# Performance work log

Hardware: AMD Instinct MI355X
Metric: run time of the kernel (lower is better)

Reference implementation:

```python
import jax, jax.numpy as jnp
import numpy as np

WINDOW = 16
NUM_HEADS = 4
DIM = 256
LN_EPS = 1e-5


def setup_inputs() -> dict:
    key = jax.random.key(0)
    ks = jax.random.split(key, 8)
    B, C, N = 8, DIM, 16384
    s = 1.0 / np.sqrt(C)
    x = jax.random.normal(ks[0], (B, C, N), dtype=jnp.float32)
    in_proj_w = jax.random.uniform(ks[1], (3 * C, C), minval=-s, maxval=s, dtype=jnp.float32)
    in_proj_b = jnp.zeros((3 * C,), dtype=jnp.float32)
    out_proj_w = jax.random.uniform(ks[2], (C, C), minval=-s, maxval=s, dtype=jnp.float32)
    out_proj_b = jnp.zeros((C,), dtype=jnp.float32)
    ln_g = jnp.ones((C,), dtype=jnp.float32)
    ln_b = jnp.zeros((C,), dtype=jnp.float32)
    return {"x": x, "in_proj_w": in_proj_w, "in_proj_b": in_proj_b,
            "out_proj_w": out_proj_w, "out_proj_b": out_proj_b,
            "ln_g": ln_g, "ln_b": ln_b}


def _swin_attn_1d(x, in_proj_w, in_proj_b, out_proj_w, out_proj_b, ln_g, ln_b):
    B, C, N = x.shape
    W = WINDOW
    H = NUM_HEADS
    hd = C // H
    xt = jnp.transpose(x, (0, 2, 1))                      # [B, N, C]
    pad_len = (W - N % W) % W                             # static Python int
    if pad_len > 0:
        xt = jnp.pad(xt, ((0, 0), (0, pad_len), (0, 0)))
    N_pad = N + pad_len
    nw = B * (N_pad // W)
    xw = xt.reshape(nw, W, C)                             # [nw, W, C]
    # QKV projection (torch MHA: x @ in_proj_w.T + in_proj_b)
    qkv = jnp.einsum('nwc,dc->nwd', xw, in_proj_w) + in_proj_b  # [nw, W, 3C]
    q, k, v = jnp.split(qkv, 3, axis=-1)
    q = q.reshape(nw, W, H, hd) * (1.0 / np.sqrt(hd))
    k = k.reshape(nw, W, H, hd)
    v = v.reshape(nw, W, H, hd)
    scores = jnp.einsum('nqhd,nkhd->nhqk', q, k)          # [nw, H, W, W]
    probs = jax.nn.softmax(scores, axis=-1)
    attn = jnp.einsum('nhqk,nkhd->nqhd', probs, v).reshape(nw, W, C)
    attn = jnp.einsum('nwc,dc->nwd', attn, out_proj_w) + out_proj_b
    # residual + LayerNorm
    y = attn + xw
    mu = jnp.mean(y, axis=-1, keepdims=True)
    var = jnp.mean(jnp.square(y - mu), axis=-1, keepdims=True)
    y = (y - mu) * jax.lax.rsqrt(var + LN_EPS) * ln_g + ln_b
    y = y.reshape(B, N_pad, C)
    if pad_len > 0:
        y = y[:, :N, :]
    return jnp.transpose(y, (0, 2, 1))                    # [B, C, N]


def reference(x, in_proj_w, in_proj_b, out_proj_w, out_proj_b, ln_g, ln_b):
    return _swin_attn_1d(x, in_proj_w, in_proj_b, out_proj_w, out_proj_b, ln_g, ln_b)
```

## Files before the change

kernel.cpp:

```cpp
#include <hip/hip_runtime.h>


#define C_DIM 256
#define NSEQ  16384

typedef __attribute__((ext_vector_type(8))) short bf16x8;
typedef __attribute__((ext_vector_type(4))) float f32x4;

__device__ __forceinline__ unsigned short f2bf(float f) {
    unsigned int u = __builtin_bit_cast(unsigned int, f);
    u += 0x7FFFu + ((u >> 16) & 1u);
    return (unsigned short)(u >> 16);
}
__device__ __forceinline__ float bf2f(unsigned short h) {
    unsigned int u = ((unsigned int)h) << 16;
    return __builtin_bit_cast(float, u);
}
__device__ __forceinline__ unsigned int pack2(float a, float b) {
    return ((unsigned int)f2bf(b) << 16) | (unsigned int)f2bf(a);
}
__device__ __forceinline__ uint2 pack4(f32x4 v) {
    uint2 r; r.x = pack2(v[0], v[1]); r.y = pack2(v[2], v[3]); return r;
}
__device__ __forceinline__ int xsw(int row, int col) {
    return col ^ (((row >> 3) & 1) << 4);
}

__global__ void prep_weights(const float* __restrict__ wq_f, const float* __restrict__ wo_f,
                             unsigned short* __restrict__ wq, unsigned short* __restrict__ wo) {
    int i = blockIdx.x * 256 + threadIdx.x;
    if (i < 768 * 256) {
        int nt = i >> 12, r = i & 4095;
        int k = r >> 9, r2 = r & 511;
        int l = r2 >> 5, r3 = r2 & 31;
        wq[i] = f2bf(wq_f[(nt * 16 + l) * 256 + k * 32 + r3]);
    }
    if (i < 256 * 256) {
        int nt = i >> 12, r = i & 4095;
        int k = r >> 9, r2 = r & 511;
        int l = r2 >> 5, r3 = r2 & 31;
        wo[i] = f2bf(wo_f[(nt * 16 + l) * 256 + k * 32 + r3]);
    }
}

__global__ __launch_bounds__(1024, 4) void swin_fused(
    const float* __restrict__ x,
    const unsigned short* __restrict__ wq,
    const unsigned short* __restrict__ wo,
    const float* __restrict__ bq,
    const float* __restrict__ bo,
    const float* __restrict__ lng,
    const float* __restrict__ lnb,
    float* __restrict__ out)
{
    __shared__ __align__(16) unsigned short lds_x[64][264];
    __shared__ __align__(16) unsigned short lds_qk[64][520];
    __shared__ __align__(16) unsigned short lds_vt[256][72];
    __shared__ __align__(16) unsigned short lds_p[16][16][16];
    __shared__ float lds_mean[64];
    __shared__ float lds_rstd[64];

    const int tid  = threadIdx.x;
    const int wv   = tid >> 6;
    const int lane = tid & 63;
    const int l15  = lane & 15;
    const int quad = lane >> 4;

    const int w0    = blockIdx.x * 4;
    const int batch = w0 >> 10;
    const int nbase = (w0 & 1023) << 4;
    const long xbase = (long)batch * ((long)C_DIM * NSEQ) + nbase;

    {
        const int t4 = (tid & 15) << 2;
        const int c4 = (tid >> 4) << 2;
        float4 r[4];
        #pragma unroll
        for (int j = 0; j < 4; ++j)
            r[j] = *reinterpret_cast<const float4*>(&x[xbase + (long)(c4 + j) * NSEQ + t4]);
        const float* rf = reinterpret_cast<const float*>(r);
        #pragma unroll
        for (int i = 0; i < 4; ++i) {
            uint2 v;
            v.x = pack2(rf[0 * 4 + i], rf[1 * 4 + i]);
            v.y = pack2(rf[2 * 4 + i], rf[3 * 4 + i]);
            *reinterpret_cast<uint2*>(&lds_x[t4 + i][xsw(t4 + i, c4)]) = v;
        }
    }

    const unsigned short* wqbase = wq + l15 * 32 + quad * 8;
    bf16x8 wA[8], wB[8];
    #pragma unroll
    for (int k = 0; k < 8; ++k)
        wA[k] = *reinterpret_cast<const bf16x8*>(wqbase + wv * 4096 + k * 512);

    __syncthreads();

    {
        #pragma unroll
        for (int k = 0; k < 8; ++k)
            wB[k] = *reinterpret_cast<const bf16x8*>(wqbase + (16 + wv) * 4096 + k * 512);
        const float4 b4 = *reinterpret_cast<const float4*>(&bq[wv * 16 + quad * 4]);
        f32x4 acc[4];
        #pragma unroll
        for (int s = 0; s < 4; ++s) acc[s] = {b4.x, b4.y, b4.z, b4.w};
        #pragma unroll
        for (int k = 0; k < 8; ++k) {
            #pragma unroll
            for (int s = 0; s < 4; ++s) {
                const int row = s * 16 + l15;
                bf16x8 a = *reinterpret_cast<const bf16x8*>(&lds_x[row][xsw(row, k * 32 + quad * 8)]);
                acc[s] = __builtin_amdgcn_mfma_f32_16x16x32_bf16(wA[k], a, acc[s], 0, 0, 0);
            }
        }
        const int cb = wv * 16 + quad * 4;
        #pragma unroll
        for (int s = 0; s < 4; ++s) {
            const int row = s * 16 + l15;
            *reinterpret_cast<uint2*>(&lds_qk[row][xsw(row, cb)]) = pack4(acc[s]);
        }
    }
    {
        #pragma unroll
        for (int k = 0; k < 8; ++k)
            wA[k] = *reinterpret_cast<const bf16x8*>(wqbase + (32 + wv) * 4096 + k * 512);
        const float4 b4 = *reinterpret_cast<const float4*>(&bq[256 + wv * 16 + quad * 4]);
        f32x4 acc[4];
        #pragma unroll
        for (int s = 0; s < 4; ++s) acc[s] = {b4.x, b4.y, b4.z, b4.w};
        #pragma unroll
        for (int k = 0; k < 8; ++k) {
            #pragma unroll
            for (int s = 0; s < 4; ++s) {
                const int row = s * 16 + l15;
                bf16x8 a = *reinterpret_cast<const bf16x8*>(&lds_x[row][xsw(row, k * 32 + quad * 8)]);
                acc[s] = __builtin_amdgcn_mfma_f32_16x16x32_bf16(wB[k], a, acc[s], 0, 0, 0);
            }
        }
        const int cb = 256 + wv * 16 + quad * 4;
        #pragma unroll
        for (int s = 0; s < 4; ++s) {
            const int row = s * 16 + l15;
            *reinterpret_cast<uint2*>(&lds_qk[row][xsw(row, cb)]) = pack4(acc[s]);
        }
    }
    {
        const float bias = bq[512 + wv * 16 + l15];
        f32x4 acc[4];
        #pragma unroll
        for (int s = 0; s < 4; ++s) acc[s] = {bias, bias, bias, bias};
        #pragma unroll
        for (int k = 0; k < 8; ++k) {
            #pragma unroll
            for (int s = 0; s < 4; ++s) {
                const int row = s * 16 + l15;
                bf16x8 a = *reinterpret_cast<const bf16x8*>(&lds_x[row][xsw(row, k * 32 + quad * 8)]);
                acc[s] = __builtin_amdgcn_mfma_f32_16x16x32_bf16(a, wA[k], acc[s], 0, 0, 0);
            }
        }
        #pragma unroll
        for (int s = 0; s < 4; ++s)
            *reinterpret_cast<uint2*>(&lds_vt[wv * 16 + l15][s * 16 + quad * 4]) = pack4(acc[s]);
    }
    __syncthreads();

    {
        const int g = wv >> 2;
        const int h = wv & 3;
        const int row = g * 16 + l15;
        f32x4 sc = {0.f, 0.f, 0.f, 0.f};
        #pragma unroll
        for (int kk = 0; kk < 2; ++kk) {
            bf16x8 aq = *reinterpret_cast<const bf16x8*>(&lds_qk[row][xsw(row, h * 64 + kk * 32 + quad * 8)]);
            bf16x8 bk = *reinterpret_cast<const bf16x8*>(&lds_qk[row][xsw(row, 256 + h * 64 + kk * 32 + quad * 8)]);
            sc = __builtin_amdgcn_mfma_f32_16x16x32_bf16(aq, bk, sc, 0, 0, 0);
        }
        #pragma unroll
        for (int r = 0; r < 4; ++r) {
            float s = sc[r] * 0.125f;
            float m = s;
            #pragma unroll
            for (int msk = 1; msk <= 8; msk <<= 1) m = fmaxf(m, __shfl_xor(m, msk, 16));
            float e = __expf(s - m);
            float su = e;
            #pragma unroll
            for (int msk = 1; msk <= 8; msk <<= 1) su += __shfl_xor(su, msk, 16);
            lds_p[wv][quad * 4 + r][l15] = f2bf(e / su);
        }
        bf16x8 ap = {0,0,0,0,0,0,0,0};
        if (quad < 2) ap = *reinterpret_cast<const bf16x8*>(&lds_p[wv][l15][quad * 8]);
        #pragma unroll
        for (int dt = 0; dt < 4; ++dt) {
            bf16x8 bv = {0,0,0,0,0,0,0,0};
            if (quad < 2)
                bv = *reinterpret_cast<const bf16x8*>(&lds_vt[h * 64 + dt * 16 + l15][g * 16 + quad * 8]);
            f32x4 acc = {0.f, 0.f, 0.f, 0.f};
            acc = __builtin_amdgcn_mfma_f32_16x16x32_bf16(bv, ap, acc, 0, 0, 0);
            const int cb = h * 64 + dt * 16 + quad * 4;
            *reinterpret_cast<uint2*>(&lds_qk[row][xsw(row, cb)]) = pack4(acc);
        }
    }

    const unsigned short* wobase = wo + l15 * 32 + quad * 8;
    #pragma unroll
    for (int k = 0; k < 8; ++k)
        wA[k] = *reinterpret_cast<const bf16x8*>(wobase + wv * 4096 + k * 512);

    __syncthreads();

    unsigned short* ldy = &lds_vt[0][0];
    {
        const float4 b4 = *reinterpret_cast<const float4*>(&bo[wv * 16 + quad * 4]);
        f32x4 acc[4];
        #pragma unroll
        for (int s = 0; s < 4; ++s) acc[s] = {b4.x, b4.y, b4.z, b4.w};
        #pragma unroll
        for (int k = 0; k < 8; ++k) {
            #pragma unroll
            for (int s = 0; s < 4; ++s) {
                const int row = s * 16 + l15;
                bf16x8 a = *reinterpret_cast<const bf16x8*>(&lds_qk[row][xsw(row, k * 32 + quad * 8)]);
                acc[s] = __builtin_amdgcn_mfma_f32_16x16x32_bf16(wA[k], a, acc[s], 0, 0, 0);
            }
        }
        const int cb = wv * 16 + quad * 4;
        #pragma unroll
        for (int s = 0; s < 4; ++s) {
            const int row = s * 16 + l15;
            uint2 xr = *reinterpret_cast<const uint2*>(&lds_x[row][xsw(row, cb)]);
            f32x4 y;
            y[0] = acc[s][0] + bf2f((unsigned short)(xr.x & 0xffff));
            y[1] = acc[s][1] + bf2f((unsigned short)(xr.x >> 16));
            y[2] = acc[s][2] + bf2f((unsigned short)(xr.y & 0xffff));
            y[3] = acc[s][3] + bf2f((unsigned short)(xr.y >> 16));
            *reinterpret_cast<uint2*>(&ldy[row * 264 + xsw(row, cb)]) = pack4(y);
        }
    }
    __syncthreads();

    {
        const int row = tid >> 4, part = tid & 15;
        float s = 0.f, sq = 0.f;
        #pragma unroll
        for (int half = 0; half < 2; ++half) {
            bf16x8 yv = *reinterpret_cast<const bf16x8*>(&ldy[row * 264 + xsw(row, part * 16 + half * 8)]);
            #pragma unroll
            for (int ii = 0; ii < 8; ++ii) {
                float v = bf2f((unsigned short)yv[ii]);
                s += v; sq += v * v;
            }
        }
        #pragma unroll
        for (int msk = 1; msk <= 8; msk <<= 1) {
            s  += __shfl_xor(s,  msk, 16);
            sq += __shfl_xor(sq, msk, 16);
        }
        if (part == 0) {
            float mean = s * (1.0f / 256.0f);
            float var  = sq * (1.0f / 256.0f) - mean * mean;
            lds_mean[row] = mean;
            lds_rstd[row] = rsqrtf(var + 1e-5f);
        }
    }
    __syncthreads();

    {
        const int t4 = (tid & 15) << 2;
        const int c0 = tid >> 4;
        float mean[4], rstd[4];
        #pragma unroll
        for (int i = 0; i < 4; ++i) { mean[i] = lds_mean[t4 + i]; rstd[i] = lds_rstd[t4 + i]; }
        #pragma unroll
        for (int it = 0; it < 4; ++it) {
            const int c = c0 + (it << 6);
            const float g = lng[c], b = lnb[c];
            float4 o;
            float* of = reinterpret_cast<float*>(&o);
            #pragma unroll
            for (int i = 0; i < 4; ++i)
                of[i] = (bf2f(ldy[(t4 + i) * 264 + xsw(t4 + i, c)]) - mean[i]) * rstd[i] * g + b;
            *reinterpret_cast<float4*>(&out[xbase + (long)c * NSEQ + t4]) = o;
        }
    }
}

extern "C" void kernel_launch(void* const* d_in, const int* in_sizes, int n_in,
                              void* d_out, int out_size, void* d_ws, size_t ws_size,
                              hipStream_t stream) {
    const float* x   = (const float*)d_in[0];
    const float* ipw = (const float*)d_in[1];
    const float* ipb = (const float*)d_in[2];
    const float* opw = (const float*)d_in[3];
    const float* opb = (const float*)d_in[4];
    const float* lng = (const float*)d_in[5];
    const float* lnb = (const float*)d_in[6];
    float* out = (float*)d_out;

    unsigned short* wq = (unsigned short*)d_ws;
    unsigned short* wo = wq + 768 * 256;

    prep_weights<<<768, 256, 0, stream>>>(ipw, opw, wq, wo);
    swin_fused<<<2048, 1024, 0, stream>>>(x, wq, wo, ipb, opb, lng, lnb, out);
}
```

Before: 352.4 us.

## Re-tile projection GEMMs so each wave keeps activation fragments in registers

Changes how the QKV and output projections are split across the 16 waves. Each wave now owns 32 rows (sp) and loops over several 16-column weight tiles (j + 8t), holding the activation fragments for its rows in registers. Before, each wave owned one weight tile and re-read all 64 rows from LDS for every k step. This cuts LDS reads of x and of the attention output, but it raises register pressure (16 bf16x8 activation fragments plus 8 weight fragments) and makes each wave reload weight tiles from global memory more often.

```diff
diff --git a/kernel.cpp b/kernel.cpp
--- a/kernel.cpp
+++ b/kernel.cpp
@@ -65,19 +65,24 @@
     const int lane = tid & 63;
     const int l15  = lane & 15;
     const int quad = lane >> 4;
+    const int sp   = wv & 1;
+    const int j    = wv >> 1;
 
     const int w0    = blockIdx.x * 4;
     const int batch = w0 >> 10;
     const int nbase = (w0 & 1023) << 4;
     const long xbase = (long)batch * ((long)C_DIM * NSEQ) + nbase;
 
+    const int rowA = sp * 32 + l15;
+    const int rowB = sp * 32 + 16 + l15;
+
     {
         const int t4 = (tid & 15) << 2;
         const int c4 = (tid >> 4) << 2;
         float4 r[4];
         #pragma unroll
-        for (int j = 0; j < 4; ++j)
-            r[j] = *reinterpret_cast<const float4*>(&x[xbase + (long)(c4 + j) * NSEQ + t4]);
+        for (int jj = 0; jj < 4; ++jj)
+            r[jj] = *reinterpret_cast<const float4*>(&x[xbase + (long)(c4 + jj) * NSEQ + t4]);
         const float* rf = reinterpret_cast<const float*>(r);
         #pragma unroll
         for (int i = 0; i < 4; ++i) {
@@ -89,78 +94,57 @@
     }
 
     const unsigned short* wqbase = wq + l15 * 32 + quad * 8;
-    bf16x8 wA[8], wB[8];
+    bf16x8 w[8];
     #pragma unroll
     for (int k = 0; k < 8; ++k)
-        wA[k] = *reinterpret_cast<const bf16x8*>(wqbase + wv * 4096 + k * 512);
-
-    __syncthreads();
-
-    {
+        w[k] = *reinterpret_cast<const bf16x8*>(wqbase + j * 4096 + k * 512);
+
+    __syncthreads();
+
+    bf16x8 xaA[8], xaB[8];
+    #pragma unroll
+    for (int k = 0; k < 8; ++k) {
+        xaA[k] = *reinterpret_cast<const bf16x8*>(&lds_x[rowA][xsw(rowA, k * 32 + quad * 8)]);
+        xaB[k] = *reinterpret_cast<const bf16x8*>(&lds_x[rowB][xsw(rowB, k * 32 + quad * 8)]);
+    }
+
+    #pragma unroll
+    for (int t = 0; t < 4; ++t) {
+        const int nt = j + 8 * t;
+        if (t) {
+            #pragma unroll
+            for (int k = 0; k < 8; ++k)
+                w[k] = *reinterpret_cast<const bf16x8*>(wqbase + nt * 4096 + k * 512);
+        }
+        const float4 b4 = *reinterpret_cast<const float4*>(&bq[nt * 16 + quad * 4]);
+        f32x4 accA = {b4.x, b4.y, b4.z, b4.w};
+        f32x4 accB = accA;
+        #pragma unroll
+        for (int k = 0; k < 8; ++k) {
+            accA = __builtin_amdgcn_mfma_f32_16x16x32_bf16(w[k], xaA[k], accA, 0, 0, 0);
+            accB = __builtin_amdgcn_mfma_f32_16x16x32_bf16(w[k], xaB[k], accB, 0, 0, 0);
+        }
+        const int cb = nt * 16 + quad * 4;
+        *reinterpret_cast<uint2*>(&lds_qk[rowA][xsw(rowA, cb)]) = pack4(accA);
+        *reinterpret_cast<uint2*>(&lds_qk[rowB][xsw(rowB, cb)]) = pack4(accB);
+    }
+    #pragma unroll
+    for (int t = 4; t < 6; ++t) {
+        const int nt = j + 8 * t;
         #pragma unroll
         for (int k = 0; k < 8; ++k)
-            wB[k] = *reinterpret_cast<const bf16x8*>(wqbase + (16 + wv) * 4096 + k * 512);
-        const float4 b4 = *reinterpret_cast<const float4*>(&bq[wv * 16 + quad * 4]);
-        f32x4 acc[4];
-        #pragma unroll
-        for (int s = 0; s < 4; ++s) acc[s] = {b4.x, b4.y, b4.z, b4.w};
+            w[k] = *reinterpret_cast<const bf16x8*>(wqbase + nt * 4096 + k * 512);
+        const float bias = bq[nt * 16 + l15];
+        f32x4 accA = {bias, bias, bias, bias};
+        f32x4 accB = accA;
         #pragma unroll
         for (int k = 0; k < 8; ++k) {
-            #pragma unroll
-            for (int s = 0; s < 4; ++s) {
-                const int row = s * 16 + l15;
-                bf16x8 a = *reinterpret_cast<const bf16x8*>(&lds_x[row][xsw(row, k * 32 + quad * 8)]);
-                acc[s] = __builtin_amdgcn_mfma_f32_16x16x32_bf16(wA[k], a, acc[s], 0, 0, 0);
-            }
-        }
-        const int cb = wv * 16 + quad * 4;
-        #pragma unroll
-        for (int s = 0; s < 4; ++s) {
-            const int row = s * 16 + l15;
-            *reinterpret_cast<uint2*>(&lds_qk[row][xsw(row, cb)]) = pack4(acc[s]);
-        }
-    }
-    {
-        #pragma unroll
-        for (int k = 0; k < 8; ++k)
-            wA[k] = *reinterpret_cast<const bf16x8*>(wqbase + (32 + wv) * 4096 + k * 512);
-        const float4 b4 = *reinterpret_cast<const float4*>(&bq[256 + wv * 16 + quad * 4]);
-        f32x4 acc[4];
-        #pragma unroll
-        for (int s = 0; s < 4; ++s) acc[s] = {b4.x, b4.y, b4.z, b4.w};
-        #pragma unroll
-        for (int k = 0; k < 8; ++k) {
-            #pragma unroll
-            for (int s = 0; s < 4; ++s) {
-                const int row = s * 16 + l15;
-                bf16x8 a = *reinterpret_cast<const bf16x8*>(&lds_x[row][xsw(row, k * 32 + quad * 8)]);
-                acc[s] = __builtin_amdgcn_mfma_f32_16x16x32_bf16(wB[k], a, acc[s], 0, 0, 0);
-            }
-        }
-        const int cb = 256 + wv * 16 + quad * 4;
-        #pragma unroll
-        for (int s = 0; s < 4; ++s) {
-            const int row = s * 16 + l15;
-            *reinterpret_cast<uint2*>(&lds_qk[row][xsw(row, cb)]) = pack4(acc[s]);
-        }
-    }
-    {
-        const float bias = bq[512 + wv * 16 + l15];
-        f32x4 acc[4];
-        #pragma unroll
-        for (int s = 0; s < 4; ++s) acc[s] = {bias, bias, bias, bias};
-        #pragma unroll
-        for (int k = 0; k < 8; ++k) {
-            #pragma unroll
-            for (int s = 0; s < 4; ++s) {
-                const int row = s * 16 + l15;
-                bf16x8 a = *reinterpret_cast<const bf16x8*>(&lds_x[row][xsw(row, k * 32 + quad * 8)]);
-                acc[s] = __builtin_amdgcn_mfma_f32_16x16x32_bf16(a, wA[k], acc[s], 0, 0, 0);
-            }
-        }
-        #pragma unroll
-        for (int s = 0; s < 4; ++s)
-            *reinterpret_cast<uint2*>(&lds_vt[wv * 16 + l15][s * 16 + quad * 4]) = pack4(acc[s]);
+            accA = __builtin_amdgcn_mfma_f32_16x16x32_bf16(xaA[k], w[k], accA, 0, 0, 0);
+            accB = __builtin_amdgcn_mfma_f32_16x16x32_bf16(xaB[k], w[k], accB, 0, 0, 0);
+        }
+        const int vr = (nt - 32) * 16 + l15;
+        *reinterpret_cast<uint2*>(&lds_vt[vr][sp * 32 + quad * 4])      = pack4(accA);
+        *reinterpret_cast<uint2*>(&lds_vt[vr][sp * 32 + 16 + quad * 4]) = pack4(accB);
     }
     __syncthreads();
 
@@ -204,36 +188,53 @@
     const unsigned short* wobase = wo + l15 * 32 + quad * 8;
     #pragma unroll
     for (int k = 0; k < 8; ++k)
-        wA[k] = *reinterpret_cast<const bf16x8*>(wobase + wv * 4096 + k * 512);
+        w[k] = *reinterpret_cast<const bf16x8*>(wobase + j * 4096 + k * 512);
 
     __syncthreads();
 
     unsigned short* ldy = &lds_vt[0][0];
     {
-        const float4 b4 = *reinterpret_cast<const float4*>(&bo[wv * 16 + quad * 4]);
-        f32x4 acc[4];
-        #pragma unroll
-        for (int s = 0; s < 4; ++s) acc[s] = {b4.x, b4.y, b4.z, b4.w};
+        bf16x8 aaA[8], aaB[8];
         #pragma unroll
         for (int k = 0; k < 8; ++k) {
-            #pragma unroll
-            for (int s = 0; s < 4; ++s) {
-                const int row = s * 16 + l15;
-                bf16x8 a = *reinterpret_cast<const bf16x8*>(&lds_qk[row][xsw(row, k * 32 + quad * 8)]);
-                acc[s] = __builtin_amdgcn_mfma_f32_16x16x32_bf16(wA[k], a, acc[s], 0, 0, 0);
-            }
-        }
-        const int cb = wv * 16 + quad * 4;
-        #pragma unroll
-        for (int s = 0; s < 4; ++s) {
-            const int row = s * 16 + l15;
-            uint2 xr = *reinterpret_cast<const uint2*>(&lds_x[row][xsw(row, cb)]);
-            f32x4 y;
-            y[0] = acc[s][0] + bf2f((unsigned short)(xr.x & 0xffff));
-            y[1] = acc[s][1] + bf2f((unsigned short)(xr.x >> 16));
-            y[2] = acc[s][2] + bf2f((unsigned short)(xr.y & 0xffff));
-            y[3] = acc[s][3] + bf2f((unsigned short)(xr.y >> 16));
-            *reinterpret_cast<uint2*>(&ldy[row * 264 + xsw(row, cb)]) = pack4(y);
+            aaA[k] = *reinterpret_cast<const bf16x8*>(&lds_qk[rowA][xsw(rowA, k * 32 + quad * 8)]);
+            aaB[k] = *reinterpret_cast<const bf16x8*>(&lds_qk[rowB][xsw(rowB, k * 32 + quad * 8)]);
+        }
+        #pragma unroll
+        for (int t = 0; t < 2; ++t) {
+            const int nt = j + 8 * t;
+            if (t) {
+                #pragma unroll
+                for (int k = 0; k < 8; ++k)
+                    w[k] = *reinterpret_cast<const bf16x8*>(wobase + nt * 4096 + k * 512);
+            }
+            const float4 b4 = *reinterpret_cast<const float4*>(&bo[nt * 16 + quad * 4]);
+            f32x4 accA = {b4.x, b4.y, b4.z, b4.w};
+            f32x4 accB = accA;
+            #pragma unroll
+            for (int k = 0; k < 8; ++k) {
+                accA = __builtin_amdgcn_mfma_f32_16x16x32_bf16(w[k], aaA[k], accA, 0, 0, 0);
+                accB = __builtin_amdgcn_mfma_f32_16x16x32_bf16(w[k], aaB[k], accB, 0, 0, 0);
+            }
+            const int cb = nt * 16 + quad * 4;
+            {
+                uint2 xr = *reinterpret_cast<const uint2*>(&lds_x[rowA][xsw(rowA, cb)]);
+                f32x4 y;
+                y[0] = accA[0] + bf2f((unsigned short)(xr.x & 0xffff));
+                y[1] = accA[1] + bf2f((unsigned short)(xr.x >> 16));
+                y[2] = accA[2] + bf2f((unsigned short)(xr.y & 0xffff));
+                y[3] = accA[3] + bf2f((unsigned short)(xr.y >> 16));
+                *reinterpret_cast<uint2*>(&ldy[rowA * 264 + xsw(rowA, cb)]) = pack4(y);
+            }
+            {
+                uint2 xr = *reinterpret_cast<const uint2*>(&lds_x[rowB][xsw(rowB, cb)]);
+                f32x4 y;
+                y[0] = accB[0] + bf2f((unsigned short)(xr.x & 0xffff));
+                y[1] = accB[1] + bf2f((unsigned short)(xr.x >> 16));
+                y[2] = accB[2] + bf2f((unsigned short)(xr.y & 0xffff));
+                y[3] = accB[3] + bf2f((unsigned short)(xr.y >> 16));
+                *reinterpret_cast<uint2*>(&ldy[rowB * 264 + xsw(rowB, cb)]) = pack4(y);
+            }
         }
     }
     __syncthreads();
```

Measured after the change: 396.1 us. +12.4%, slower.
